# Optimization experiments

Measured on AMD Instinct MI355X. Metric: run time of the kernel, lower is better.

The kernel has to match this reference:

```python
import jax, jax.numpy as jnp
import numpy as np

D_MODEL = 256
N_HEAD = 4
N_LAYERS = 2
D_FF = 4 * D_MODEL
VOCAB = 4096
DINO = 384
T_SEQ = 40
N_PATCH = 256
B = 32
LN_EPS = 1e-5


def setup_inputs() -> dict:
    key = jax.random.key(0)
    ks = jax.random.split(key, 24)
    f = jnp.float32
    d = {}
    d['patches'] = jax.random.normal(ks[0], (B, N_PATCH, DINO), dtype=f)
    d['tokens'] = jax.random.randint(ks[1], (B, T_SEQ), 0, VOCAB)
    s = 0.02
    d['embedding'] = jax.random.normal(ks[2], (VOCAB, D_MODEL), dtype=f) * s
    d['pos_emb'] = jax.random.normal(ks[3], (T_SEQ, D_MODEL), dtype=f) * s
    d['in_proj_w'] = jax.random.normal(ks[4], (N_LAYERS, 3 * D_MODEL, D_MODEL), dtype=f) * s
    d['in_proj_b'] = jnp.zeros((N_LAYERS, 3 * D_MODEL), dtype=f)
    d['out_proj_w'] = jax.random.normal(ks[5], (N_LAYERS, D_MODEL, D_MODEL), dtype=f) * s
    d['out_proj_b'] = jnp.zeros((N_LAYERS, D_MODEL), dtype=f)
    d['lin1_w'] = jax.random.normal(ks[6], (N_LAYERS, D_FF, D_MODEL), dtype=f) * s
    d['lin1_b'] = jnp.zeros((N_LAYERS, D_FF), dtype=f)
    d['lin2_w'] = jax.random.normal(ks[7], (N_LAYERS, D_MODEL, D_FF), dtype=f) * s
    d['lin2_b'] = jnp.zeros((N_LAYERS, D_MODEL), dtype=f)
    d['ln1_g'] = jnp.ones((N_LAYERS, D_MODEL), dtype=f)
    d['ln1_b'] = jnp.zeros((N_LAYERS, D_MODEL), dtype=f)
    d['ln2_g'] = jnp.ones((N_LAYERS, D_MODEL), dtype=f)
    d['ln2_b'] = jnp.zeros((N_LAYERS, D_MODEL), dtype=f)
    d['fus_w1'] = jax.random.normal(ks[8], (D_MODEL, DINO + D_MODEL), dtype=f) * s
    d['fus_b1'] = jnp.zeros((D_MODEL,), dtype=f)
    d['fus_w2'] = jax.random.normal(ks[9], (D_MODEL, D_MODEL), dtype=f) * s
    d['fus_b2'] = jnp.zeros((D_MODEL,), dtype=f)
    d['cls_w'] = jax.random.normal(ks[10], (VOCAB, D_MODEL), dtype=f) * s
    d['cls_b'] = jnp.zeros((VOCAB,), dtype=f)
    return d


def _layer_norm(x, g, b):
    m = jnp.mean(x, axis=-1, keepdims=True)
    v = jnp.mean((x - m) ** 2, axis=-1, keepdims=True)
    return (x - m) / jnp.sqrt(v + LN_EPS) * g + b


def _encode(x, mask, in_proj_w, in_proj_b, out_proj_w, out_proj_b,
            lin1_w, lin1_b, lin2_w, lin2_b, ln1_g, ln1_b, ln2_g, ln2_b):
    # x: [N, S, d], mask: [N, S] bool (True = valid key). Post-norm encoder, relu FFN.
    N, S, d = x.shape
    hd = d // N_HEAD
    for i in range(N_LAYERS):
        qkv = x @ in_proj_w[i].T + in_proj_b[i]
        q, k, v = jnp.split(qkv, 3, axis=-1)
        sh = lambda t: t.reshape(N, S, N_HEAD, hd).transpose(0, 2, 1, 3)
        q, k, v = sh(q), sh(k), sh(v)
        sc = jnp.einsum('nhqd,nhkd->nhqk', q, k) / np.sqrt(hd)
        sc = jnp.where(mask[:, None, None, :], sc, -1e9)
        a = jax.nn.softmax(sc, axis=-1)
        o = jnp.einsum('nhqk,nhkd->nhqd', a, v).transpose(0, 2, 1, 3).reshape(N, S, d)
        o = o @ out_proj_w[i].T + out_proj_b[i]
        x = _layer_norm(x + o, ln1_g[i], ln1_b[i])
        ff = jax.nn.relu(x @ lin1_w[i].T + lin1_b[i]) @ lin2_w[i].T + lin2_b[i]
        x = _layer_norm(x + ff, ln2_g[i], ln2_b[i])
    return x


def reference(patches, tokens, embedding, pos_emb, in_proj_w, in_proj_b,
              out_proj_w, out_proj_b, lin1_w, lin1_b, lin2_w, lin2_b,
              ln1_g, ln1_b, ln2_g, ln2_b, fus_w1, fus_b1, fus_w2, fus_b2,
              cls_w, cls_b):
    Bsz, T = tokens.shape
    d = embedding.shape[1]
    emb = embedding[tokens] + pos_emb[None, :T, :]      # [B, T, d]
    Tm1 = T - 1
    # All 39 prefix runs at once: prefix of length t+1 == full seq with keys > t masked.
    X = jnp.broadcast_to(emb[None], (Tm1, Bsz, T, d)).reshape(Tm1 * Bsz, T, d)
    valid = jnp.arange(T)[None, :] <= jnp.arange(Tm1)[:, None]  # [Tm1, T]
    mask = jnp.broadcast_to(valid[:, None, :], (Tm1, Bsz, T)).reshape(Tm1 * Bsz, T)
    enc = _encode(X, mask, in_proj_w, in_proj_b, out_proj_w, out_proj_b,
                  lin1_w, lin1_b, lin2_w, lin2_b, ln1_g, ln1_b, ln2_g, ln2_b)
    enc = enc.reshape(Tm1, Bsz, T, d)
    idx = jnp.arange(Tm1)
    ctx_rest = enc[idx, :, idx, :]                      # [Tm1, B, d] last valid position
    ctx = jnp.concatenate([jnp.zeros((1, Bsz, d), emb.dtype), ctx_rest], axis=0)  # [T, B, d]
    # Fusion MLP: split first linear into patch part (t-invariant) + context part.
    w1p, w1c = fus_w1[:, :DINO], fus_w1[:, DINO:]
    pp = jnp.einsum('bpd,kd->bpk', patches, w1p)        # [B, P, d]
    cp = jnp.einsum('tbd,kd->tbk', ctx, w1c) + fus_b1   # [T, B, d]
    h = jax.nn.gelu(pp[None] + cp[:, :, None, :], approximate=False)  # [T, B, P, d]
    feat = jnp.einsum('tbpk,mk->tbpm', h, fus_w2) + fus_b2            # [T, B, P, d]
    # Gather-only classification: prob of tokens[:, t] at step t.
    targets = tokens.T                                   # [T, B]
    cw = cls_w[targets]                                  # [T, B, d]
    cb = cls_b[targets]                                  # [T, B]
    logits = jnp.einsum('tbpm,tbm->tbp', feat, cw) + cb[:, :, None]
    probs = jax.nn.sigmoid(logits)                       # [T, B, P]
    return probs.transpose(1, 2, 0)                      # [B, P, T]
```

## Files before the change

### kernel.cpp

```cpp
#include <hip/hip_runtime.h>
#include <math.h>

#define DM    256
#define NH    4
#define HD    64
#define TS    40
#define TM1   39
#define BB    32
#define DFF   1024
#define DINO  384
#define NPATCH 256
#define VOCAB 4096

#define NTOK  24960
#define NQ2   1248

typedef _Float16 f16;
typedef __attribute__((ext_vector_type(8))) _Float16 half8;
typedef __attribute__((ext_vector_type(4))) _Float16 half4;
typedef __attribute__((ext_vector_type(4))) float f32x4;

#define OFF_EMBH   0u
#define OFF_EMB    163840u
#define OFF_QKVH   491520u
#define OFF_X1     983040u
#define OFF_X1H    7372800u
#define OFF_H1     10567680u
#define OFF_BIG    16957440u
#define   BT_AO1H  6389760u
#define   BT_X2    6553600u
#define   BT_X2H   6881280u
#define   BT_FF2H  7045120u
#define   BT_H1H   7700480u
#define OFF_CTX    29736960u
#define OFF_CPB    30064640u
#define OFF_U      30392320u
#define OFF_S      30720000u
#define OFF_WQKVH  30722048u
#define OFF_WQ1H   30820352u
#define OFF_KVWH   30853120u
#define OFF_WOH    30918656u
#define OFF_WOH1   30951424u
#define OFF_L1WH   30984192u
#define OFF_L1WH1  31115264u
#define OFF_L2WH   31246336u
#define OFF_L2WH1  31377408u
#define OFF_W1PH   31508480u
#define OFF_W1CH   31557632u
#define OFF_FW2TH  31590400u
#define OFF_CWGH   31623168u
#define OFF_MAP    31787008u
#define WS_FLOATS  31813216u

__global__ __launch_bounds__(256) void prep_kernel(
    const int* __restrict__ tokens, const float* __restrict__ etab,
    const float* __restrict__ pos,
    const float* __restrict__ ipw, const float* __restrict__ opw,
    const float* __restrict__ l1w, const float* __restrict__ l2w,
    const float* __restrict__ fw1, const float* __restrict__ fw2,
    const float* __restrict__ clsw, const float* __restrict__ clsb,
    const float* __restrict__ fb2,
    float* __restrict__ emb, f16* __restrict__ embh,
    f16* __restrict__ wqkvh, f16* __restrict__ wq1h, f16* __restrict__ kvwh,
    f16* __restrict__ woh, f16* __restrict__ woh1,
    f16* __restrict__ l1wh, f16* __restrict__ l1wh1,
    f16* __restrict__ l2wh, f16* __restrict__ l2wh1,
    f16* __restrict__ w1ph, f16* __restrict__ w1ch, f16* __restrict__ fw2th,
    f16* __restrict__ cwgh, float* __restrict__ sv, float* __restrict__ ctx,
    int* __restrict__ map1, int* __restrict__ map2)
{
    int i = blockIdx.x * 256 + threadIdx.x;
    if (i < 327680) {
        int r = i >> 8, j = i & 255;
        int p = r % TS;
        float v = etab[(size_t)tokens[r] * DM + j] + pos[p * DM + j];
        emb[i] = v; embh[i] = (f16)v;
        return;
    }
    i -= 327680;
    if (i < 196608) { wqkvh[i] = (f16)ipw[i]; return; }
    i -= 196608;
    if (i < 65536)  { wq1h[i] = (f16)ipw[196608 + i]; return; }
    i -= 65536;
    if (i < 131072) { kvwh[i] = (f16)ipw[262144 + i]; return; }
    i -= 131072;
    if (i < 65536)  { woh[i]  = (f16)opw[i]; return; }
    i -= 65536;
    if (i < 65536)  { woh1[i] = (f16)opw[65536 + i]; return; }
    i -= 65536;
    if (i < 262144) { l1wh[i]  = (f16)l1w[i]; return; }
    i -= 262144;
    if (i < 262144) { l1wh1[i] = (f16)l1w[262144 + i]; return; }
    i -= 262144;
    if (i < 262144) { l2wh[i]  = (f16)l2w[i]; return; }
    i -= 262144;
    if (i < 262144) { l2wh1[i] = (f16)l2w[262144 + i]; return; }
    i -= 262144;
    if (i < 98304) {
        int r = i / 384, c = i - r * 384;
        w1ph[i] = (f16)fw1[r * 640 + c];
        return;
    }
    i -= 98304;
    if (i < 65536) {
        int n = i >> 8, k = i & 255;
        w1ch[i] = (f16)fw1[n * 640 + 384 + k];
        return;
    }
    i -= 65536;
    if (i < 65536) {
        int j = i >> 8, k = i & 255;
        fw2th[i] = (f16)fw2[k * 256 + j];
        return;
    }
    i -= 65536;
    if (i < 327680) {
        int tb = i >> 8, j = i & 255;
        int t = tb >> 5, b = tb & 31;
        cwgh[i] = (f16)clsw[(size_t)tokens[b * TS + t] * DM + j];
        return;
    }
    i -= 327680;
    if (i < 81920) {
        int tb = i >> 6, l = i & 63;
        int t = tb >> 5, b = tb & 31;
        int tok = tokens[b * TS + t];
        float a = 0.f;
#pragma unroll
        for (int c = 0; c < 4; ++c)
            a += fb2[l + 64 * c] * clsw[(size_t)tok * DM + l + 64 * c];
#pragma unroll
        for (int o = 32; o; o >>= 1) a += __shfl_xor(a, o);
        if (l == 0) sv[tb] = a + clsb[tok];
        return;
    }
    i -= 81920;
    if (i < 8192) { ctx[i] = 0.f; return; }
    i -= 8192;
    if (i < NQ2) {
        int t = i >> 5, b = i & 31;
        map2[i] = ((t * (t + 1)) / 2 + t) * 32 + b;
    }
    if (i < NTOK) {
        int q = i >> 5, b = i & 31;
        int t = 0;
        while (((t + 1) * (t + 2)) / 2 <= q) ++t;
        int p = q - (t * (t + 1)) / 2;
        map1[i] = b * TS + p;
    }
}

__device__ __forceinline__ void stage16(const f16* g, f16* lbase_wave_uniform) {
    __builtin_amdgcn_global_load_lds(
        (const __attribute__((address_space(1))) void*)g,
        (__attribute__((address_space(3))) void*)lbase_wave_uniform, 16, 0, 0);
}

__device__ __forceinline__ half8 load_frag8(const float* p) {
    float4 a0 = *(const float4*)p;
    float4 a1 = *(const float4*)(p + 4);
    half8 h;
    h[0] = (f16)a0.x; h[1] = (f16)a0.y; h[2] = (f16)a0.z; h[3] = (f16)a0.w;
    h[4] = (f16)a1.x; h[5] = (f16)a1.y; h[6] = (f16)a1.z; h[7] = (f16)a1.w;
    return h;
}

template <int BM, typename TA, bool RELU, bool OUTF16>
__global__ __launch_bounds__(256) void gemm_x(
    const TA* __restrict__ A, int lda,
    const f16* __restrict__ B, int ldb,
    const float* __restrict__ bias,
    void* __restrict__ Cv, int ldc, int K)
{
    constexpr int AF  = BM / 8;
    constexpr int TF  = AF + 16;
    constexpr int MRE = BM / 32;
    constexpr int LPW = TF / 4;
    constexpr bool ASYNC = __is_same(TA, f16);
    constexpr int NBUF = ASYNC ? 2 : 1;
    __shared__ __align__(16) f16 lds[NBUF * TF * 512];
    int tid = threadIdx.x;
    int w = tid >> 6, l = tid & 63;
    int m0 = blockIdx.y * BM, n0 = blockIdx.x << 7;
    int lrow = l & 15;
    int lk8  = (l >> 4) << 3;
    int wm = w >> 1, wn = w & 1;

    f32x4 acc[MRE][4] = {};

    auto stage = [&](f16* dst, int k0) {
#pragma unroll
        for (int j = 0; j < TF / 4; ++j) {
            int f = (j << 2) | w;
            if (f < AF) {
                int mi = f >> 1, kc = f & 1;
                const TA* ga = A + (size_t)(m0 + (mi << 4) + lrow) * lda + k0 + (kc << 5) + lk8;
                if constexpr (ASYNC) {
                    stage16((const f16*)ga, dst + (f << 9));
                } else {
                    *(half8*)&dst[(f << 9) + (l << 3)] = load_frag8((const float*)ga);
                }
            } else {
                int fb = f - AF;
                int nj = fb >> 1, kc = fb & 1;
                const f16* gb = B + (size_t)(n0 + (nj << 4) + lrow) * ldb + k0 + (kc << 5) + lk8;
                stage16(gb, dst + (f << 9));
            }
        }
    };

    auto compute = [&](const f16* buf) {
#pragma unroll
        for (int kc = 0; kc < 2; ++kc) {
            half8 af[MRE], bfr[4];
#pragma unroll
            for (int i = 0; i < MRE; ++i)
                af[i] = *(const half8*)&buf[((((wm * MRE + i) << 1) | kc) << 9) + (l << 3)];
#pragma unroll
            for (int j2 = 0; j2 < 4; ++j2)
                bfr[j2] = *(const half8*)&buf[((AF + ((((wn << 2) | j2) << 1) | kc)) << 9) + (l << 3)];
#pragma unroll
            for (int i = 0; i < MRE; ++i)
#pragma unroll
                for (int j2 = 0; j2 < 4; ++j2)
                    acc[i][j2] = __builtin_amdgcn_mfma_f32_16x16x32_f16(
                        af[i], bfr[j2], acc[i][j2], 0, 0, 0);
        }
    };

    if constexpr (ASYNC) {
        int nk = K >> 6;
        stage(lds, 0);
        for (int t = 0; t < nk; ++t) {
            f16* cur = lds + (t & 1) * (TF * 512);
            if (t + 1 < nk) {
                stage(lds + ((t + 1) & 1) * (TF * 512), (t + 1) << 6);
                asm volatile("s_waitcnt vmcnt(%0)" :: "i"(LPW) : "memory");
            } else {
                asm volatile("s_waitcnt vmcnt(0)" ::: "memory");
            }
            __builtin_amdgcn_s_barrier();
            asm volatile("" ::: "memory");
            compute(cur);
            asm volatile("" ::: "memory");
            __builtin_amdgcn_s_barrier();
            asm volatile("" ::: "memory");
        }
    } else {
        for (int k0 = 0; k0 < K; k0 += 64) {
            stage(lds, k0);
            __syncthreads();
            compute(lds);
            __syncthreads();
        }
    }

    int colq = l & 15, rowq = (l >> 4) << 2;
#pragma unroll
    for (int i = 0; i < MRE; ++i) {
        int gmb = m0 + (wm * MRE + i) * 16 + rowq;
#pragma unroll
        for (int j2 = 0; j2 < 4; ++j2) {
            int gn = n0 + ((wn << 2) | j2) * 16 + colq;
            float bv = bias ? bias[gn] : 0.f;
#pragma unroll
            for (int r = 0; r < 4; ++r) {
                float v = acc[i][j2][r] + bv;
                if (RELU) v = fmaxf(v, 0.f);
                if (OUTF16)
                    ((f16*)Cv)[(size_t)(gmb + r) * ldc + gn] = (f16)v;
                else
                    ((float*)Cv)[(size_t)(gmb + r) * ldc + gn] = v;
            }
        }
    }
}

__global__ __launch_bounds__(256) void ln_kernel(
    float* __restrict__ X, const float* __restrict__ res,
    const int* __restrict__ map, const float* __restrict__ g,
    const float* __restrict__ beta, int nrows, f16* __restrict__ outh)
{
    int r = blockIdx.x * 4 + (threadIdx.x >> 6);
    if (r >= nrows) return;
    int l = threadIdx.x & 63;
    float* xp = X + (size_t)r * DM + l * 4;
    float4 v = *(float4*)xp;
    if (res) {
        int rr = map ? map[r] : r;
        float4 rv = *(const float4*)(res + (size_t)rr * DM + l * 4);
        v.x += rv.x; v.y += rv.y; v.z += rv.z; v.w += rv.w;
    }
    float s = v.x + v.y + v.z + v.w;
#pragma unroll
    for (int o = 32; o; o >>= 1) s += __shfl_xor(s, o);
    float mean = s * (1.f / 256.f);
    float dx = v.x - mean, dy = v.y - mean, dz = v.z - mean, dw = v.w - mean;
    float s2 = dx * dx + dy * dy + dz * dz + dw * dw;
#pragma unroll
    for (int o = 32; o; o >>= 1) s2 += __shfl_xor(s2, o);
    float rstd = 1.f / sqrtf(s2 * (1.f / 256.f) + 1e-5f);
    float4 gv = *(const float4*)(g + l * 4);
    float4 bv = *(const float4*)(beta + l * 4);
    float4 ov;
    ov.x = dx * rstd * gv.x + bv.x;
    ov.y = dy * rstd * gv.y + bv.y;
    ov.z = dz * rstd * gv.z + bv.z;
    ov.w = dw * rstd * gv.w + bv.w;
    *(float4*)xp = ov;
    if (outh) {
        half4 oh;
        oh[0] = (f16)ov.x; oh[1] = (f16)ov.y; oh[2] = (f16)ov.z; oh[3] = (f16)ov.w;
        *(half4*)(outh + (size_t)r * DM + l * 4) = oh;
    }
}

__global__ __launch_bounds__(256) void attn0_kernel(
    const f16* __restrict__ qkv, f16* __restrict__ ao)
{
    int bp = blockIdx.x;
    int b = bp / 39, p = bp % 39;
    int tid = threadIdx.x;
    int h = tid >> 6, l = tid & 63;

    float qv = (float)qkv[(size_t)(b * TS + p) * 768 + h * 64 + l];

    int krow = (l < 39) ? l : 38;
    const f16* Kr = qkv + (size_t)(b * TS + krow) * 768 + 256 + h * 64;
    float acc = 0.f;
#pragma unroll
    for (int c = 0; c < 8; ++c) {
        half8 k8 = *(const half8*)(Kr + c * 8);
#pragma unroll
        for (int j = 0; j < 8; ++j)
            acc += __shfl(qv, c * 8 + j) * (float)k8[j];
    }
    float s = acc * 0.125f;

    float m = -1e30f, lsum = 0.f, o = 0.f;
    for (int t = p; t < TM1; ++t) {
        float st = __shfl(s, t);
        float mnew = fmaxf(m, st);
        float c = __expf(m - mnew);
        float e = __expf(st - mnew);
        lsum = lsum * c + e;
        float vv = (float)qkv[(size_t)(b * TS + t) * 768 + 512 + h * 64 + l];
        o = o * c + e * vv;
        m = mnew;
        int row = ((t * (t + 1)) >> 1) + p;
        ao[((size_t)row * 32 + b) * DM + h * 64 + l] = (f16)(o / lsum);
    }
}

__global__ __launch_bounds__(256) void attn1_kernel(
    const float* __restrict__ h1, const f16* __restrict__ kv1,
    const f16* __restrict__ Wq, const float* __restrict__ bq,
    f16* __restrict__ ao1)
{
    int tb = blockIdx.x;
    int t = tb >> 5, b = tb & 31;
    int tid = threadIdx.x;
    int h = tid >> 6, l = tid & 63;
    int tri = (t * (t + 1)) >> 1;
    __shared__ float h1r[DM];
    h1r[tid] = h1[((size_t)(tri + t) * 32 + b) * DM + tid];
    __syncthreads();

    float q = bq[h * 64 + l];
    const half8* w8 = (const half8*)(Wq + (size_t)(h * 64 + l) * DM);
#pragma unroll 8
    for (int c = 0; c < 32; ++c) {
        half8 ww = w8[c];
#pragma unroll
        for (int j = 0; j < 8; ++j)
            q += (float)ww[j] * h1r[c * 8 + j];
    }

    int kr = (l <= t) ? l : t;
    const f16* Kp = kv1 + ((size_t)(tri + kr) * 32 + b) * 512 + h * 64;
    float sc = 0.f;
#pragma unroll
    for (int c = 0; c < 8; ++c) {
        half8 k8 = *(const half8*)(Kp + c * 8);
#pragma unroll
        for (int j = 0; j < 8; ++j)
            sc += __shfl(q, c * 8 + j) * (float)k8[j];
    }
    sc = (l <= t) ? sc * 0.125f : -1e30f;
    float m = sc;
#pragma unroll
    for (int o = 32; o; o >>= 1) m = fmaxf(m, __shfl_xor(m, o));
    float e = (l <= t) ? __expf(sc - m) : 0.f;
    float ss = e;
#pragma unroll
    for (int o = 32; o; o >>= 1) ss += __shfl_xor(ss, o);
    float a = e / ss;

    float o = 0.f;
    for (int k = 0; k <= t; ++k) {
        float ak = __shfl(a, k);
        o += ak * (float)kv1[((size_t)(tri + k) * 32 + b) * 512 + 256 + h * 64 + l];
    }
    ao1[(size_t)tb * DM + h * 64 + l] = (f16)o;
}

__device__ __forceinline__ float gelu_f(float x)
{
    float ax = fabsf(x);
    float z  = ax * 0.70710678118654752440f;
    float d  = 1.f + z * (0.278393f + z * (0.230389f + z * (0.000972f + z * 0.078108f)));
    float d2 = d * d;
    float E  = 1.f - __builtin_amdgcn_rcpf(d2 * d2);
    return 0.5f * x + 0.5f * ax * E;
}

__global__ __launch_bounds__(256) void final_out(
    const f16* __restrict__ pp, const float* __restrict__ cpb,
    const float* __restrict__ u, const float* __restrict__ sv,
    float* __restrict__ out)
{
    int blk = blockIdx.x;
    int b  = blk / 20;
    int rr = blk - b * 20;
    int pg = rr / 5;
    int tg = rr - pg * 5;
    int tid = threadIdx.x;
    int w = tid >> 6, l = tid & 63;

    __shared__ unsigned ldsT[128 * 64];

    {
        const f16* rowp = pp + (size_t)((b << 8) + (pg << 6) + l) * DM + (w << 6);
#pragma unroll
        for (int j = 0; j < 8; ++j) {
            half8 h8 = *(const half8*)(rowp + j * 8);
#pragma unroll
            for (int j2 = 0; j2 < 4; ++j2) {
                union { f16 h[2]; unsigned v; } cv;
                cv.h[0] = h8[j2 * 2]; cv.h[1] = h8[j2 * 2 + 1];
                int k2 = (w << 5) + (j << 2) + j2;
                ldsT[(k2 << 6) + l] = cv.v;
            }
        }
    }
    __syncthreads();

    int t0  = tg * 8 + w * 2;
    int tb0 = __builtin_amdgcn_readfirstlane(t0 * 32 + b);
    int tb1 = tb0 + 32;
    const float* cpa = cpb + (size_t)tb0 * DM;
    const float* cpc = cpb + (size_t)tb1 * DM;
    const float* ua  = u + (size_t)tb0 * DM;
    const float* uc  = u + (size_t)tb1 * DM;

    float acc0 = 0.f, acc1 = 0.f;
#pragma unroll 4
    for (int k2 = 0; k2 < 128; ++k2) {
        union { unsigned v; f16 h[2]; } pr;
        pr.v = ldsT[(k2 << 6) + l];
        float a0 = (float)pr.h[0], a1 = (float)pr.h[1];
        float2 c0 = *(const float2*)(cpa + (k2 << 1));
        float2 c1 = *(const float2*)(cpc + (k2 << 1));
        float2 u0 = *(const float2*)(ua + (k2 << 1));
        float2 u1 = *(const float2*)(uc + (k2 << 1));
        acc0 += gelu_f(a0 + c0.x) * u0.x + gelu_f(a1 + c0.y) * u0.y;
        acc1 += gelu_f(a0 + c1.x) * u1.x + gelu_f(a1 + c1.y) * u1.y;
    }
    float s0 = sv[tb0], s1 = sv[tb1];
    int op = ((b << 8) + (pg << 6) + l) * TS;
    out[op + t0]     = 1.f / (1.f + __expf(-(acc0 + s0)));
    out[op + t0 + 1] = 1.f / (1.f + __expf(-(acc1 + s1)));
}

extern "C" void kernel_launch(void* const* d_in, const int* in_sizes, int n_in,
                              void* d_out, int out_size, void* d_ws, size_t ws_size,
                              hipStream_t stream)
{
    (void)in_sizes; (void)n_in; (void)out_size;
    const float* patches   = (const float*)d_in[0];
    const int*   tokens    = (const int*)  d_in[1];
    const float* embedding = (const float*)d_in[2];
    const float* pos_emb   = (const float*)d_in[3];
    const float* in_proj_w = (const float*)d_in[4];
    const float* in_proj_b = (const float*)d_in[5];
    const float* out_proj_w= (const float*)d_in[6];
    const float* out_proj_b= (const float*)d_in[7];
    const float* lin1_w    = (const float*)d_in[8];
    const float* lin1_b    = (const float*)d_in[9];
    const float* lin2_w    = (const float*)d_in[10];
    const float* lin2_b    = (const float*)d_in[11];
    const float* ln1_g     = (const float*)d_in[12];
    const float* ln1_b     = (const float*)d_in[13];
    const float* ln2_g     = (const float*)d_in[14];
    const float* ln2_b     = (const float*)d_in[15];
    const float* fus_w1    = (const float*)d_in[16];
    const float* fus_b1    = (const float*)d_in[17];
    const float* fus_w2    = (const float*)d_in[18];
    const float* fus_b2    = (const float*)d_in[19];
    const float* cls_w     = (const float*)d_in[20];
    const float* cls_b     = (const float*)d_in[21];

    if (ws_size < (size_t)WS_FLOATS * 4) return;

    float* ws   = (float*)d_ws;
    f16*   embh = (f16*)(ws + OFF_EMBH);
    float* emb  = ws + OFF_EMB;
    f16*   qkvh = (f16*)(ws + OFF_QKVH);
    float* x1   = ws + OFF_X1;
    f16*   x1h  = (f16*)(ws + OFF_X1H);
    f16*   pph  = (f16*)(ws + OFF_X1H);
    float* h1   = ws + OFF_H1;
    float* big  = ws + OFF_BIG;
    f16*   ao0h = (f16*)big;
    f16*   ff1h = (f16*)big;
    f16*   kv1h = (f16*)big;
    f16*   ao1h = (f16*)(big + BT_AO1H);
    float* x2   = big + BT_X2;
    f16*   x2h  = (f16*)(big + BT_X2H);
    f16*   ff2h = (f16*)(big + BT_FF2H);
    f16*   h1h  = (f16*)(big + BT_H1H);
    float* ctx  = ws + OFF_CTX;
    float* cpb  = ws + OFF_CPB;
    float* u    = ws + OFF_U;
    float* svec = ws + OFF_S;
    f16*   wqkvh= (f16*)(ws + OFF_WQKVH);
    f16*   wq1h = (f16*)(ws + OFF_WQ1H);
    f16*   kvwh = (f16*)(ws + OFF_KVWH);
    f16*   woh  = (f16*)(ws + OFF_WOH);
    f16*   woh1 = (f16*)(ws + OFF_WOH1);
    f16*   l1wh = (f16*)(ws + OFF_L1WH);
    f16*   l1wh1= (f16*)(ws + OFF_L1WH1);
    f16*   l2wh = (f16*)(ws + OFF_L2WH);
    f16*   l2wh1= (f16*)(ws + OFF_L2WH1);
    f16*   w1ph = (f16*)(ws + OFF_W1PH);
    f16*   w1ch = (f16*)(ws + OFF_W1CH);
    f16*   fw2th= (f16*)(ws + OFF_FW2TH);
    f16*   cwgh = (f16*)(ws + OFF_CWGH);
    int*   map1 = (int*)(ws + OFF_MAP);
    int*   map2 = map1 + NTOK;

    prep_kernel<<<10050, 256, 0, stream>>>(
        tokens, embedding, pos_emb, in_proj_w, out_proj_w, lin1_w, lin2_w,
        fus_w1, fus_w2, cls_w, cls_b, fus_b2,
        emb, embh, wqkvh, wq1h, kvwh, woh, woh1, l1wh, l1wh1, l2wh, l2wh1,
        w1ph, w1ch, fw2th, cwgh, svec, ctx, map1, map2);

    gemm_x<64, f16, false, false><<<dim3(2, 20), 256, 0, stream>>>(
        cwgh, DM, fw2th, DM, nullptr, u, DM, DM);

    gemm_x<64, f16, false, true><<<dim3(6, 20), 256, 0, stream>>>(
        embh, DM, wqkvh, DM, in_proj_b, qkvh, 768, DM);
    attn0_kernel<<<NQ2, 256, 0, stream>>>(qkvh, ao0h);
    gemm_x<64, f16, false, false><<<dim3(2, 390), 256, 0, stream>>>(
        ao0h, DM, woh, DM, out_proj_b, x1, DM, DM);
    ln_kernel<<<6240, 256, 0, stream>>>(x1, emb, map1, ln1_g, ln1_b, NTOK, x1h);
    gemm_x<128, f16, true, true><<<dim3(8, 195), 256, 0, stream>>>(
        x1h, DM, l1wh, DM, lin1_b, ff1h, DFF, DM);
    gemm_x<64, f16, false, false><<<dim3(2, 390), 256, 0, stream>>>(
        ff1h, DFF, l2wh, DFF, lin2_b, h1, DM, DFF);
    ln_kernel<<<6240, 256, 0, stream>>>(h1, x1, nullptr, ln2_g, ln2_b, NTOK, h1h);

    gemm_x<64, float, false, true><<<dim3(2, 128), 256, 0, stream>>>(
        patches, DINO, w1ph, DINO, nullptr, pph, DM, DINO);

    gemm_x<128, f16, false, true><<<dim3(4, 195), 256, 0, stream>>>(
        h1h, DM, kvwh, DM, in_proj_b + 768 + 256, kv1h, 512, DM);
    attn1_kernel<<<NQ2, 256, 0, stream>>>(
        h1, kv1h, wq1h, in_proj_b + 768, ao1h);
    gemm_x<64, f16, false, false><<<dim3(2, 20), 256, 0, stream>>>(
        ao1h, DM, woh1, DM, out_proj_b + DM, x2, DM, DM);
    ln_kernel<<<312, 256, 0, stream>>>(x2, h1, map2, ln1_g + DM, ln1_b + DM, NQ2, x2h);
    gemm_x<64, f16, true, true><<<dim3(8, 20), 256, 0, stream>>>(
        x2h, DM, l1wh1, DM, lin1_b + DFF, ff2h, DFF, DM);
    gemm_x<64, f16, false, false><<<dim3(2, 20), 256, 0, stream>>>(
        ff2h, DFF, l2wh1, DFF, lin2_b + DM, ctx + BB * DM, DM, DFF);
    ln_kernel<<<312, 256, 0, stream>>>(ctx + BB * DM, x2, nullptr, ln2_g + DM, ln2_b + DM, NQ2, nullptr);

    gemm_x<64, float, false, false><<<dim3(2, 20), 256, 0, stream>>>(
        ctx, DM, w1ch, DM, fus_b1, cpb, DM, DM);

    final_out<<<640, 256, 0, stream>>>(pph, cpb, u, svec, (float*)d_out);
}
```

Before: 444.8 us.

## Fuse FFN lin1+ReLU+lin2 into one kernel keeping hidden activations in LDS

Adds a fused_ff kernel that computes the FFN for a 64-row tile. It stages the input rows in shared memory, computes each 128-wide chunk of the ReLU hidden layer into LDS, and accumulates the second GEMM in registers. This removes the 24960x1024 f16 intermediate round-trip through global memory and two kernel launches per layer. In exchange, weights are read directly from global memory without LDS staging, and the grid drops to 390 blocks (20 for layer 2), which lowers parallelism and may cause redundant weight traffic.

Measured after the change: 525.7 us. +18.2%, slower.

```diff
diff --git a/kernel.cpp b/kernel.cpp
--- a/kernel.cpp
+++ b/kernel.cpp
@@ -276,6 +276,101 @@
     }
 }
 
+__global__ __launch_bounds__(256) void fused_ff(
+    const f16* __restrict__ A, const f16* __restrict__ W1,
+    const f16* __restrict__ W2, const float* __restrict__ b1,
+    const float* __restrict__ b2, float* __restrict__ out)
+{
+    __shared__ __align__(16) f16 alds[32 * 512];
+    __shared__ __align__(16) f16 ffb[64 * 136];
+    int tid = threadIdx.x;
+    int w = tid >> 6, l = tid & 63;
+    int m0 = blockIdx.x << 6;
+    int lrow = l & 15, lk8 = (l >> 4) << 3;
+    int wm = w >> 1, wn = w & 1;
+    int colq = l & 15, rowq = (l >> 4) << 2;
+
+#pragma unroll
+    for (int j = 0; j < 8; ++j) {
+        int f = (j << 2) | w;
+        int mi = f >> 3, kc = f & 7;
+        stage16(A + (size_t)(m0 + (mi << 4) + lrow) * DM + (kc << 5) + lk8,
+                &alds[f << 9]);
+    }
+    __syncthreads();
+
+    f32x4 acc2[2][8] = {};
+
+    for (int j = 0; j < 8; ++j) {
+        f32x4 acc1[2][4] = {};
+#pragma unroll
+        for (int kc = 0; kc < 8; ++kc) {
+            half8 af[2], bf[4];
+#pragma unroll
+            for (int i = 0; i < 2; ++i)
+                af[i] = *(const half8*)&alds[((((((wm << 1) | i) << 3) | kc) << 9)) + (l << 3)];
+#pragma unroll
+            for (int n = 0; n < 4; ++n) {
+                int w1r = (j << 7) + (wn << 6) + (n << 4) + lrow;
+                bf[n] = *(const half8*)(W1 + (size_t)w1r * DM + (kc << 5) + lk8);
+            }
+#pragma unroll
+            for (int i = 0; i < 2; ++i)
+#pragma unroll
+                for (int n = 0; n < 4; ++n)
+                    acc1[i][n] = __builtin_amdgcn_mfma_f32_16x16x32_f16(
+                        af[i], bf[n], acc1[i][n], 0, 0, 0);
+        }
+#pragma unroll
+        for (int i = 0; i < 2; ++i) {
+            int row = (wm << 5) + (i << 4) + rowq;
+#pragma unroll
+            for (int n = 0; n < 4; ++n) {
+                int col = (wn << 6) + (n << 4) + colq;
+                float bv = b1[(j << 7) + col];
+#pragma unroll
+                for (int r = 0; r < 4; ++r)
+                    ffb[(row + r) * 136 + col] = (f16)fmaxf(acc1[i][n][r] + bv, 0.f);
+            }
+        }
+        __syncthreads();
+#pragma unroll
+        for (int kc2 = 0; kc2 < 4; ++kc2) {
+            half8 a2[2], b2f[8];
+#pragma unroll
+            for (int i = 0; i < 2; ++i) {
+                int row = (wm << 5) + (i << 4) + lrow;
+                a2[i] = *(const half8*)&ffb[row * 136 + (kc2 << 5) + lk8];
+            }
+#pragma unroll
+            for (int n = 0; n < 8; ++n) {
+                int w2r = (wn << 7) + (n << 4) + lrow;
+                b2f[n] = *(const half8*)(W2 + (size_t)w2r * DFF + (j << 7) + (kc2 << 5) + lk8);
+            }
+#pragma unroll
+            for (int i = 0; i < 2; ++i)
+#pragma unroll
+                for (int n = 0; n < 8; ++n)
+                    acc2[i][n] = __builtin_amdgcn_mfma_f32_16x16x32_f16(
+                        a2[i], b2f[n], acc2[i][n], 0, 0, 0);
+        }
+        __syncthreads();
+    }
+
+#pragma unroll
+    for (int i = 0; i < 2; ++i) {
+        int gm = m0 + (wm << 5) + (i << 4) + rowq;
+#pragma unroll
+        for (int n = 0; n < 8; ++n) {
+            int gn = (wn << 7) + (n << 4) + colq;
+            float bv = b2[gn];
+#pragma unroll
+            for (int r = 0; r < 4; ++r)
+                out[(size_t)(gm + r) * DM + gn] = acc2[i][n][r] + bv;
+        }
+    }
+}
+
 __global__ __launch_bounds__(256) void ln_kernel(
     float* __restrict__ X, const float* __restrict__ res,
     const int* __restrict__ map, const float* __restrict__ g,
@@ -512,12 +607,10 @@
     float* h1   = ws + OFF_H1;
     float* big  = ws + OFF_BIG;
     f16*   ao0h = (f16*)big;
-    f16*   ff1h = (f16*)big;
     f16*   kv1h = (f16*)big;
     f16*   ao1h = (f16*)(big + BT_AO1H);
     float* x2   = big + BT_X2;
     f16*   x2h  = (f16*)(big + BT_X2H);
-    f16*   ff2h = (f16*)(big + BT_FF2H);
     f16*   h1h  = (f16*)(big + BT_H1H);
     float* ctx  = ws + OFF_CTX;
     float* cpb  = ws + OFF_CPB;
@@ -554,10 +647,7 @@
     gemm_x<64, f16, false, false><<<dim3(2, 390), 256, 0, stream>>>(
         ao0h, DM, woh, DM, out_proj_b, x1, DM, DM);
     ln_kernel<<<6240, 256, 0, stream>>>(x1, emb, map1, ln1_g, ln1_b, NTOK, x1h);
-    gemm_x<128, f16, true, true><<<dim3(8, 195), 256, 0, stream>>>(
-        x1h, DM, l1wh, DM, lin1_b, ff1h, DFF, DM);
-    gemm_x<64, f16, false, false><<<dim3(2, 390), 256, 0, stream>>>(
-        ff1h, DFF, l2wh, DFF, lin2_b, h1, DM, DFF);
+    fused_ff<<<390, 256, 0, stream>>>(x1h, l1wh, l2wh, lin1_b, lin2_b, h1);
     ln_kernel<<<6240, 256, 0, stream>>>(h1, x1, nullptr, ln2_g, ln2_b, NTOK, h1h);
 
     gemm_x<64, float, false, true><<<dim3(2, 128), 256, 0, stream>>>(
@@ -570,10 +660,8 @@
     gemm_x<64, f16, false, false><<<dim3(2, 20), 256, 0, stream>>>(
         ao1h, DM, woh1, DM, out_proj_b + DM, x2, DM, DM);
     ln_kernel<<<312, 256, 0, stream>>>(x2, h1, map2, ln1_g + DM, ln1_b + DM, NQ2, x2h);
-    gemm_x<64, f16, true, true><<<dim3(8, 20), 256, 0, stream>>>(
-        x2h, DM, l1wh1, DM, lin1_b + DFF, ff2h, DFF, DM);
-    gemm_x<64, f16, false, false><<<dim3(2, 20), 256, 0, stream>>>(
-        ff2h, DFF, l2wh1, DFF, lin2_b + DM, ctx + BB * DM, DM, DFF);
+    fused_ff<<<20, 256, 0, stream>>>(x2h, l1wh1, l2wh1, lin1_b + DFF, lin2_b + DM,
+                                     ctx + BB * DM);
     ln_kernel<<<312, 256, 0, stream>>>(ctx + BB * DM, x2, nullptr, ln2_g + DM, ln2_b + DM, NQ2, nullptr);
 
     gemm_x<64, float, false, false><<<dim3(2, 20), 256, 0, stream>>>(
```
